# Optimization experiments

Measured on AMD Instinct MI355X. Metric: run time of the kernel, lower is better.

The kernel has to match this reference:

```python
import jax, jax.numpy as jnp
import numpy as np

B, IN, H, T = 4096, 1024, 1024, 12
TIME_PENALTY = 0.01
PONDER_EPS = 0.01


def lstm_cell(x, h, c, Wih, Whh, bih, bhh):
    # PyTorch LSTMCell: gates ordered i, f, g, o
    g = x @ Wih.T + bih + h @ Whh.T + bhh  # [B, 4H]
    i, f, gg, o = jnp.split(g, 4, axis=1)
    i = jax.nn.sigmoid(i)
    f = jax.nn.sigmoid(f)
    gg = jnp.tanh(gg)
    o = jax.nn.sigmoid(o)
    c_new = f * c + i * gg
    h_new = o * jnp.tanh(c_new)
    return h_new, c_new


def setup_inputs() -> dict:
    key = jax.random.key(0)
    ks = jax.random.split(key, 12)
    k1 = 1.0 / np.sqrt(H)
    u = lambda k, shape: jax.random.uniform(k, shape, jnp.float32, -k1, k1)
    return {
        "inputs": jax.random.normal(ks[0], (B, IN), jnp.float32),
        "W_ih1": u(ks[1], (4 * H, IN + 1)),
        "W_hh1": u(ks[2], (4 * H, H)),
        "b_ih1": u(ks[3], (4 * H,)),
        "b_hh1": u(ks[4], (4 * H,)),
        "W_ih2": u(ks[5], (4 * H, H)),
        "W_hh2": u(ks[6], (4 * H, H)),
        "b_ih2": u(ks[7], (4 * H,)),
        "b_hh2": u(ks[8], (4 * H,)),
        "W_halt": u(ks[9], (1, H)),
        "b_halt": jnp.full((1,), -1.0, jnp.float32),  # initial_halting_bias
    }


def reference(inputs, W_ih1, W_hh1, b_ih1, b_hh1, W_ih2, W_hh2, b_ih2, b_hh2, W_halt, b_halt):
    batch = inputs.shape[0]
    budget = jnp.float32(1.0 - PONDER_EPS)

    h1 = jnp.zeros((batch, H), jnp.float32)
    c1 = jnp.zeros((batch, H), jnp.float32)
    h2 = jnp.zeros((batch, H), jnp.float32)
    c2 = jnp.zeros((batch, H), jnp.float32)
    halt_accum = jnp.zeros((batch, 1), jnp.float32)
    acc_out = jnp.zeros((batch, H), jnp.float32)
    acc_rem = jnp.zeros((batch, 1), jnp.float32)
    ponder_steps = jnp.zeros((batch,), jnp.float32)
    cont = jnp.ones((batch, 1), bool)
    is_first = jnp.array(True)

    def step(carry, _):
        h1, c1, h2, c2, halt_accum, acc_out, acc_rem, ponder_steps, cont, is_first = carry
        active = jnp.any(cont)  # mimic torch's early break: inactive steps are no-ops
        flag = jnp.where(is_first, 1.0, 0.0) * jnp.ones((batch, 1), jnp.float32)
        x = jnp.concatenate([inputs, flag], axis=1)
        h1n, c1n = lstm_cell(x, h1, c1, W_ih1, W_hh1, b_ih1, b_hh1)
        act = jax.nn.relu(h1n)
        h2n, c2n = lstm_cell(act, h2, c2, W_ih2, W_hh2, b_ih2, b_hh2)
        step_halt = jax.nn.sigmoid(h2n @ W_halt.T + b_halt)  # [B,1]
        cont_f = cont.astype(jnp.float32)
        masked_halt = step_halt * cont_f
        halt_n = halt_accum + masked_halt
        ending = (halt_n > budget) & cont
        cont_n = cont & jnp.logical_not(ending)
        masked_rem = ending.astype(jnp.float32) * (1.0 - halt_n)
        acc_out_n = acc_out + (masked_halt + masked_rem) * h2n
        acc_rem_n = acc_rem + masked_halt
        ponder_n = ponder_steps + cont_n[:, 0].astype(jnp.float32)
        sel = lambda new, old: jnp.where(active, new, old)
        carry_n = (sel(h1n, h1), sel(c1n, c1), sel(h2n, h2), sel(c2n, c2),
                   sel(halt_n, halt_accum), sel(acc_out_n, acc_out),
                   sel(acc_rem_n, acc_rem), sel(ponder_n, ponder_steps),
                   jnp.where(active, cont_n, cont),
                   is_first & jnp.logical_not(active))
        return carry_n, None

    carry = (h1, c1, h2, c2, halt_accum, acc_out, acc_rem, ponder_steps, cont, is_first)
    carry, _ = jax.lax.scan(step, carry, None, length=T)
    h1, c1, h2, c2, halt_accum, acc_out, acc_rem, ponder_steps, cont, _ = carry

    # for-else branch: samples still continuing after time_limit get the remainder
    acc_out = acc_out + cont.astype(jnp.float32) * (1.0 - halt_accum) * h2
    ponder_cost = -1.0 * TIME_PENALTY * jnp.mean(acc_rem)
    return acc_out, h1, c1, h2, c2, ponder_cost, ponder_steps
```

## Files before the change

kernel.cpp:

```cpp
#include <hip/hip_runtime.h>
#include <cstdint>
#include <cstddef>


typedef _Float16 f16;
typedef f16   f16x8 __attribute__((ext_vector_type(8)));
typedef f16   f16x4 __attribute__((ext_vector_type(4)));
typedef float f32x4 __attribute__((ext_vector_type(4)));

#define TSTEPS 12

#define O_ACC   0u
#define O_H1    4194304u
#define O_C1    8388608u
#define O_H2    12582912u
#define O_C2    16777216u
#define O_PCOST 20971520u
#define O_PSTEP 20971521u

#define WS_C1    (size_t)(0u)
#define WS_C2    ((size_t)16u<<20)
#define WS_H1HI0 ((size_t)32u<<20)
#define WS_H1HI1 ((size_t)40u<<20)
#define WS_H1LO0 ((size_t)48u<<20)
#define WS_H1LO1 ((size_t)56u<<20)
#define WS_H2HI0 ((size_t)64u<<20)
#define WS_H2HI1 ((size_t)72u<<20)
#define WS_H2LO0 ((size_t)80u<<20)
#define WS_H2LO1 ((size_t)88u<<20)
#define WS_ACTHI ((size_t)96u<<20)
#define WS_ACTLO ((size_t)104u<<20)
#define WS_MISC  ((size_t)112u<<20)

#define SEC_AHI 0
#define SEC_ALO 16384
#define SEC_BHI 32768
#define SEC_BLO 49152
#define BUFSZ   65536

__device__ __forceinline__ float sigmoidf_(float x) { return 1.0f / (1.0f + expf(-x)); }

__device__ __forceinline__ void glds16(const void* g, void* l) {
    __builtin_amdgcn_global_load_lds(
        (const __attribute__((address_space(1))) unsigned int*)g,
        (__attribute__((address_space(3))) unsigned int*)l, 16, 0, 0);
}

__device__ __forceinline__ void block_tile(int& m0, int& hc0) {
    const int bid = blockIdx.x;
    const int lid = (bid & 7) * 32 + (bid >> 3);
    m0  = (lid & 15) * 256;
    hc0 = (lid >> 4) * 64;
}

template<bool B_PAIR>
__device__ __forceinline__ void pass256(
    const f16* __restrict__ Ahi, const f16* __restrict__ Alo,
    const f16* __restrict__ Bhi, const f16* __restrict__ Blo,
    const float* __restrict__ Bf32,
    int m0, int hc0, f32x4 (&acc)[8][4], char* sm)
{
    const int tid = threadIdx.x, lane = tid & 63, wid = tid >> 6;
    const int wm  = (wid >> 2) * 128;
    const int wnb = wid & 3;
    const int l15 = lane & 15, lk = lane >> 4;

    int aoff[8], boff[4];
#pragma unroll
    for (int mf = 0; mf < 8; ++mf) {
        const int row = wm + mf * 16 + l15;
        aoff[mf] = row * 64 + ((lk ^ (((row >> 1) ^ (row >> 3)) & 3)) << 4);
    }
#pragma unroll
    for (int nf = 0; nf < 4; ++nf) {
        const int lv = wnb * 64 + nf * 16 + l15;
        boff[nf] = lv * 64 + ((lk ^ (((lv >> 1) ^ (lv >> 3)) & 3)) << 4);
    }

    constexpr int NOPS = B_PAIR ? 8 : 4;
    const f16* gsrc[NOPS];
    int ldst[NOPS];
    {
        const int gl_d = lane >> 2;
        const int sl   = lane & 3;
        const int swz_gd = ((gl_d >> 1) ^ (gl_d >> 3)) & 3;
#pragma unroll
        for (int i = 0; i < NOPS; ++i) {
            const int o = wid * NOPS + i;
            const int sec = o >> 4, j = o & 15;
            const int swzv = (swz_gd ^ (2 * j)) & 3;
            const f16* base;
            size_t row;
            if (sec <= 1) { base = (sec == 0) ? Ahi : Alo; row = (size_t)(m0 + 16 * j + gl_d); }
            else {
                base = (sec == 2) ? Bhi : Blo;
                row = (size_t)((j & 3) * 1024 + hc0 + (j >> 2) * 16 + gl_d);
            }
            gsrc[i] = base + row * 1024 + ((sl ^ swzv) << 3);
            ldst[i] = sec * 16384 + j * 1024 + lane * 16;
        }
    }

    const int blv = tid >> 1;
    const int bswz = ((blv >> 1) ^ (blv >> 3)) & 3;
    const float* bsrc = nullptr;
    float4 breg[4];
    if constexpr (!B_PAIR) {
        const int wrow = ((blv >> 4) & 3) * 1024 + hc0 + (blv >> 6) * 16 + (blv & 15);
        bsrc = Bf32 + (size_t)wrow * 1024 + (tid & 1) * 16;
    }

    auto issue = [&](int i, int kt, char* buf) {
        glds16(gsrc[i] + kt * 32, buf + ldst[i]);
    };
    auto loadB = [&](int kt) {
#pragma unroll
        for (int i = 0; i < 4; ++i) breg[i] = *(const float4*)(bsrc + kt * 32 + i * 4);
    };
    auto writeB = [&](char* buf) {
#pragma unroll
        for (int i2 = 0; i2 < 2; ++i2) {
            const float4 va = breg[2 * i2], vb = breg[2 * i2 + 1];
            const f16 h0 = (f16)va.x, h1 = (f16)va.y, h2 = (f16)va.z, h3 = (f16)va.w;
            const f16 h4 = (f16)vb.x, h5 = (f16)vb.y, h6 = (f16)vb.z, h7 = (f16)vb.w;
            const f16x8 hv = {h0, h1, h2, h3, h4, h5, h6, h7};
            const f16x8 lw = {(f16)(va.x - (float)h0), (f16)(va.y - (float)h1),
                              (f16)(va.z - (float)h2), (f16)(va.w - (float)h3),
                              (f16)(vb.x - (float)h4), (f16)(vb.y - (float)h5),
                              (f16)(vb.z - (float)h6), (f16)(vb.w - (float)h7)};
            const int slot = ((tid & 1) * 2 + i2) ^ bswz;
            const int off = blv * 64 + (slot << 4);
            *(f16x8*)(buf + SEC_BHI + off) = hv;
            *(f16x8*)(buf + SEC_BLO + off) = lw;
        }
    };

    constexpr int IST_P[5] = {0, 3, 6, 8, 8};
    constexpr int IST_M[5] = {0, 2, 3, 4, 4};

#pragma unroll
    for (int i = 0; i < NOPS; ++i) issue(i, 0, sm);
    if constexpr (!B_PAIR) {
        loadB(0);
        asm volatile("s_waitcnt vmcnt(0)" ::: "memory");
        writeB(sm);
    }
    asm volatile("s_waitcnt vmcnt(0) lgkmcnt(0)" ::: "memory");
    __builtin_amdgcn_s_barrier();
    asm volatile("" ::: "memory");

    int cur = 0;
#pragma unroll 1
    for (int kt = 0; kt < 32; ++kt) {
        char* bc = sm + cur * BUFSZ;
        char* bn = sm + (cur ^ 1) * BUFSZ;
        const bool pre = (kt < 31);
        f16x8 bh[4], bl[4];
#pragma unroll
        for (int p = 0; p < 4; ++p) {
            f16x8 ah0 = *(const f16x8*)(bc + SEC_AHI + aoff[2 * p]);
            f16x8 ah1 = *(const f16x8*)(bc + SEC_AHI + aoff[2 * p + 1]);
            f16x8 al0 = *(const f16x8*)(bc + SEC_ALO + aoff[2 * p]);
            f16x8 al1 = *(const f16x8*)(bc + SEC_ALO + aoff[2 * p + 1]);
            if (p == 0) {
#pragma unroll
                for (int nf = 0; nf < 4; ++nf) {
                    bh[nf] = *(const f16x8*)(bc + SEC_BHI + boff[nf]);
                    bl[nf] = *(const f16x8*)(bc + SEC_BLO + boff[nf]);
                }
            }
            if (pre) {
                if constexpr (B_PAIR) {
#pragma unroll
                    for (int i = IST_P[p]; i < IST_P[p + 1]; ++i) issue(i, kt + 1, bn);
                } else {
#pragma unroll
                    for (int i = IST_M[p]; i < IST_M[p + 1]; ++i) issue(i, kt + 1, bn);
                    if (p == 0) loadB(kt + 1);
                }
            }
            __builtin_amdgcn_s_barrier();
            __builtin_amdgcn_s_setprio(1);
#pragma unroll
            for (int i = 0; i < 2; ++i) {
                const f16x8 xh = i ? ah1 : ah0;
                const f16x8 xl = i ? al1 : al0;
#pragma unroll
                for (int nf = 0; nf < 4; ++nf) {
                    acc[2 * p + i][nf] = __builtin_amdgcn_mfma_f32_16x16x32_f16(xh, bh[nf], acc[2 * p + i][nf], 0, 0, 0);
                    acc[2 * p + i][nf] = __builtin_amdgcn_mfma_f32_16x16x32_f16(xh, bl[nf], acc[2 * p + i][nf], 0, 0, 0);
                    acc[2 * p + i][nf] = __builtin_amdgcn_mfma_f32_16x16x32_f16(xl, bh[nf], acc[2 * p + i][nf], 0, 0, 0);
                }
            }
            __builtin_amdgcn_s_setprio(0);
            if (p < 3) __builtin_amdgcn_s_barrier();
        }
        asm volatile("s_waitcnt vmcnt(0)" ::: "memory");
        if constexpr (!B_PAIR) { if (pre) writeB(bn); }
        asm volatile("s_waitcnt lgkmcnt(0)" ::: "memory");
        __builtin_amdgcn_s_barrier();
        asm volatile("" ::: "memory");
        cur ^= 1;
    }
}

__global__ __launch_bounds__(512) void k_z1(
    const f16* __restrict__ xhi, const f16* __restrict__ xlo,
    const f16* __restrict__ W1hi, const f16* __restrict__ W1lo,
    const float* __restrict__ bih1, const float* __restrict__ bhh1,
    float* __restrict__ Z1)
{
    __shared__ __align__(16) char sm[2 * BUFSZ];
    int m0, hc0; block_tile(m0, hc0);
    f32x4 acc[8][4];
#pragma unroll
    for (int a = 0; a < 8; ++a)
#pragma unroll
        for (int b = 0; b < 4; ++b) acc[a][b] = (f32x4){0.f, 0.f, 0.f, 0.f};
    pass256<true>(xhi, xlo, W1hi, W1lo, nullptr, m0, hc0, acc, sm);

    const int tid = threadIdx.x, lane = tid & 63, wid = tid >> 6;
    const int wm = (wid >> 2) * 128, wnb = wid & 3, l15 = lane & 15, lk = lane >> 4;
    const int hc = hc0 + wnb * 16 + l15;
#pragma unroll
    for (int mf = 0; mf < 8; ++mf)
#pragma unroll
        for (int r = 0; r < 4; ++r) {
            const int row = m0 + wm + mf * 16 + lk * 4 + r;
#pragma unroll
            for (int g = 0; g < 4; ++g) {
                const int R = g * 1024 + hc;
                Z1[(size_t)row * 4096 + R] = acc[mf][g][r] + bih1[R] + bhh1[R];
            }
        }
}

__global__ __launch_bounds__(512) void k_stepA(
    const float* __restrict__ Z1, const float* __restrict__ Whh1,
    const f16* __restrict__ h1hi_in, const f16* __restrict__ h1lo_in,
    const float* __restrict__ flagcol, float* __restrict__ c1,
    f16* __restrict__ h1hi_out, f16* __restrict__ h1lo_out,
    f16* __restrict__ acthi, f16* __restrict__ actlo,
    const unsigned* __restrict__ cnt_prev, int step)
{
    if (step > 0 && cnt_prev[0] == 0u) return;
    __shared__ __align__(16) char sm[2 * BUFSZ];
    int m0, hc0; block_tile(m0, hc0);
    f32x4 acc[8][4];
#pragma unroll
    for (int a = 0; a < 8; ++a)
#pragma unroll
        for (int b = 0; b < 4; ++b) acc[a][b] = (f32x4){0.f, 0.f, 0.f, 0.f};
    if (step > 0)
        pass256<false>(h1hi_in, h1lo_in, nullptr, nullptr, Whh1, m0, hc0, acc, sm);

    const int tid = threadIdx.x, lane = tid & 63, wid = tid >> 6;
    const int wm = (wid >> 2) * 128, wnb = wid & 3, l15 = lane & 15, lk = lane >> 4;
    const int hc = hc0 + wnb * 16 + l15;
#pragma unroll
    for (int mf = 0; mf < 8; ++mf)
#pragma unroll
        for (int r = 0; r < 4; ++r) {
            const int row = m0 + wm + mf * 16 + lk * 4 + r;
            float p[4];
#pragma unroll
            for (int g = 0; g < 4; ++g) {
                const int R = g * 1024 + hc;
                p[g] = acc[mf][g][r] + Z1[(size_t)row * 4096 + R];
                if (step == 0) p[g] += flagcol[R];
            }
            const float ig = sigmoidf_(p[0]);
            const float fg = sigmoidf_(p[1]);
            const float gg = tanhf(p[2]);
            const float og = sigmoidf_(p[3]);
            const int idx = row * 1024 + hc;
            const float cold = (step == 0) ? 0.0f : c1[idx];
            const float cn = fg * cold + ig * gg;
            c1[idx] = cn;
            const float h = og * tanhf(cn);
            const f16 hh = (f16)h;
            const f16 hl = (f16)(h - (float)hh);
            h1hi_out[idx] = hh; h1lo_out[idx] = hl;
            const bool pos = h > 0.0f;
            acthi[idx] = pos ? hh : (f16)0.0f;
            actlo[idx] = pos ? hl : (f16)0.0f;
        }
}

__global__ __launch_bounds__(512) void k_stepB(
    const f16* __restrict__ acthi, const f16* __restrict__ actlo,
    const float* __restrict__ Wih2,
    const f16* __restrict__ h2hi_in, const f16* __restrict__ h2lo_in,
    const float* __restrict__ Whh2,
    const float* __restrict__ bih2, const float* __restrict__ bhh2,
    float* __restrict__ c2, f16* __restrict__ h2hi_out, f16* __restrict__ h2lo_out,
    const unsigned* __restrict__ cnt_prev, int step)
{
    if (step > 0 && cnt_prev[0] == 0u) return;
    __shared__ __align__(16) char sm[2 * BUFSZ];
    int m0, hc0; block_tile(m0, hc0);
    f32x4 acc[8][4];
#pragma unroll
    for (int a = 0; a < 8; ++a)
#pragma unroll
        for (int b = 0; b < 4; ++b) acc[a][b] = (f32x4){0.f, 0.f, 0.f, 0.f};
    pass256<false>(acthi, actlo, nullptr, nullptr, Wih2, m0, hc0, acc, sm);
    if (step > 0)
        pass256<false>(h2hi_in, h2lo_in, nullptr, nullptr, Whh2, m0, hc0, acc, sm);

    const int tid = threadIdx.x, lane = tid & 63, wid = tid >> 6;
    const int wm = (wid >> 2) * 128, wnb = wid & 3, l15 = lane & 15, lk = lane >> 4;
    const int hc = hc0 + wnb * 16 + l15;
#pragma unroll
    for (int mf = 0; mf < 8; ++mf)
#pragma unroll
        for (int r = 0; r < 4; ++r) {
            const int row = m0 + wm + mf * 16 + lk * 4 + r;
            float p[4];
#pragma unroll
            for (int g = 0; g < 4; ++g) {
                const int R = g * 1024 + hc;
                p[g] = acc[mf][g][r] + bih2[R] + bhh2[R];
            }
            const float ig = sigmoidf_(p[0]);
            const float fg = sigmoidf_(p[1]);
            const float gg = tanhf(p[2]);
            const float og = sigmoidf_(p[3]);
            const int idx = row * 1024 + hc;
            const float cold = (step == 0) ? 0.0f : c2[idx];
            const float cn = fg * cold + ig * gg;
            c2[idx] = cn;
            const float h = og * tanhf(cn);
            const f16 hh = (f16)h;
            h2hi_out[idx] = hh;
            h2lo_out[idx] = (f16)(h - (float)hh);
        }
}

__global__ __launch_bounds__(256) void k_haltacc(
    const f16* __restrict__ h2hi, const f16* __restrict__ h2lo,
    const float* __restrict__ Whalt, const float* __restrict__ bhalt,
    float* __restrict__ halt, float* __restrict__ cont,
    float* __restrict__ ponder_out, unsigned* __restrict__ ctrl,
    float* __restrict__ acc_out,
    const unsigned* __restrict__ cnt_prev, int step)
{
    if (step > 0 && cnt_prev[0] == 0u) return;
    const int lane = threadIdx.x & 63;
    const int b = blockIdx.x * 4 + (threadIdx.x >> 6);
    const size_t base = (size_t)b * 1024;
    float sum = 0.0f;
    for (int k = lane; k < 1024; k += 64)
        sum += ((float)h2hi[base + k] + (float)h2lo[base + k]) * Whalt[k];
#pragma unroll
    for (int off = 32; off > 0; off >>= 1) sum += __shfl_down(sum, off, 64);
    float co = 0.0f;
    if (lane == 0) {
        const float sh = sigmoidf_(sum + bhalt[0]);
        if (cont[b] != 0.0f) {
            const float hn = halt[b] + sh;
            const bool ending = hn > 0.99f;
            co = sh + (ending ? (1.0f - hn) : 0.0f);
            halt[b] = hn;
            if (!ending) {
                ponder_out[b] += 1.0f;
                atomicAdd(&ctrl[step], 1u);
            } else {
                cont[b] = 0.0f;
            }
        }
        if (b == 0) ctrl[12] = (unsigned)(step + 1);
    }
    co = __shfl(co, 0, 64);
    if (step == 0 || co != 0.0f) {
        float4* dst = (float4*)(acc_out + base);
        const f16x4* hi4 = (const f16x4*)(h2hi + base);
        const f16x4* lo4 = (const f16x4*)(h2lo + base);
#pragma unroll
        for (int j = 0; j < 4; ++j) {
            const int i = lane + 64 * j;
            const f16x4 hv = hi4[i];
            const f16x4 lv = lo4[i];
            float4 d = (step == 0) ? (float4){0.f, 0.f, 0.f, 0.f} : dst[i];
            d.x = fmaf(co, (float)hv[0] + (float)lv[0], d.x);
            d.y = fmaf(co, (float)hv[1] + (float)lv[1], d.y);
            d.z = fmaf(co, (float)hv[2] + (float)lv[2], d.z);
            d.w = fmaf(co, (float)hv[3] + (float)lv[3], d.w);
            dst[i] = d;
        }
    }
}

__global__ __launch_bounds__(256) void k_small_init(
    float* __restrict__ halt, float* __restrict__ cont,
    float* __restrict__ ponder_out, unsigned* __restrict__ ctrl)
{
    const int b = blockIdx.x * 256 + threadIdx.x;
    if (b < 4096) { halt[b] = 0.0f; cont[b] = 1.0f; ponder_out[b] = 0.0f; }
    if (b < 16) ctrl[b] = 0u;
}

__global__ __launch_bounds__(256) void k_split_flat(
    const float* __restrict__ src, f16* __restrict__ hi, f16* __restrict__ lo)
{
    const size_t i = ((size_t)blockIdx.x * 256 + threadIdx.x) * 4;
    const float4 v = *(const float4*)(src + i);
    const f16 s0 = (f16)v.x, s1 = (f16)v.y, s2 = (f16)v.z, s3 = (f16)v.w;
    const f16x4 hv = {s0, s1, s2, s3};
    const f16x4 lw = {(f16)(v.x - (float)s0), (f16)(v.y - (float)s1),
                      (f16)(v.z - (float)s2), (f16)(v.w - (float)s3)};
    *(f16x4*)(hi + i) = hv;
    *(f16x4*)(lo + i) = lw;
}

__global__ __launch_bounds__(256) void k_split_wih1(
    const float* __restrict__ src, f16* __restrict__ hi, f16* __restrict__ lo,
    float* __restrict__ flagcol)
{
    const int t = blockIdx.x * 256 + threadIdx.x;
    const int row = t >> 8, c4 = (t & 255) << 2;
    const float* s = src + (size_t)row * 1025 + c4;
    const float v0 = s[0], v1 = s[1], v2 = s[2], v3 = s[3];
    const f16 s0 = (f16)v0, s1 = (f16)v1, s2 = (f16)v2, s3 = (f16)v3;
    const f16x4 hv = {s0, s1, s2, s3};
    const f16x4 lw = {(f16)(v0 - (float)s0), (f16)(v1 - (float)s1),
                      (f16)(v2 - (float)s2), (f16)(v3 - (float)s3)};
    const size_t di = (size_t)row * 1024 + c4;
    *(f16x4*)(hi + di) = hv;
    *(f16x4*)(lo + di) = lw;
    if ((t & 255) == 0) flagcol[row] = src[(size_t)row * 1025 + 1024];
}

__global__ __launch_bounds__(256) void k_fin1(
    const f16* __restrict__ h1hi0, const f16* __restrict__ h1hi1,
    const f16* __restrict__ h1lo0, const f16* __restrict__ h1lo1,
    const f16* __restrict__ h2hi0, const f16* __restrict__ h2hi1,
    const f16* __restrict__ h2lo0, const f16* __restrict__ h2lo1,
    const float* __restrict__ c1s, const float* __restrict__ c2s,
    const float* __restrict__ halt, const float* __restrict__ cont,
    const unsigned* __restrict__ ctrl, float* __restrict__ out)
{
    const int par = (int)(ctrl[12] & 1u);
    const f16* h1h = par ? h1hi1 : h1hi0;
    const f16* h1l = par ? h1lo1 : h1lo0;
    const f16* h2h = par ? h2hi1 : h2hi0;
    const f16* h2l = par ? h2lo1 : h2lo0;
    const int b = blockIdx.x;
    const float rem = (cont[b] != 0.0f) ? (1.0f - halt[b]) : 0.0f;
    const int base = b * 1024;
    for (int i = threadIdx.x; i < 1024; i += 256) {
        const float h1v = (float)h1h[base + i] + (float)h1l[base + i];
        const float h2v = (float)h2h[base + i] + (float)h2l[base + i];
        out[O_H1 + base + i] = h1v;
        out[O_C1 + base + i] = c1s[base + i];
        out[O_H2 + base + i] = h2v;
        out[O_C2 + base + i] = c2s[base + i];
        if (rem != 0.0f) out[O_ACC + base + i] += rem * h2v;
    }
}

__global__ __launch_bounds__(256) void k_fin2(
    const float* __restrict__ halt, float* __restrict__ out)
{
    __shared__ float red[256];
    float s = 0.0f;
    for (int i = threadIdx.x; i < 4096; i += 256) s += halt[i];
    red[threadIdx.x] = s;
    __syncthreads();
    for (int w = 128; w > 0; w >>= 1) {
        if (threadIdx.x < w) red[threadIdx.x] += red[threadIdx.x + w];
        __syncthreads();
    }
    if (threadIdx.x == 0) out[O_PCOST] = -0.01f * (red[0] * (1.0f / 4096.0f));
}

extern "C" void kernel_launch(void* const* d_in, const int* in_sizes, int n_in,
                              void* d_out, int out_size, void* d_ws, size_t ws_size,
                              hipStream_t stream) {
    const float* inputs = (const float*)d_in[0];
    const float* W_ih1  = (const float*)d_in[1];
    const float* W_hh1  = (const float*)d_in[2];
    const float* b_ih1  = (const float*)d_in[3];
    const float* b_hh1  = (const float*)d_in[4];
    const float* W_ih2  = (const float*)d_in[5];
    const float* W_hh2  = (const float*)d_in[6];
    const float* b_ih2  = (const float*)d_in[7];
    const float* b_hh2  = (const float*)d_in[8];
    const float* W_halt = (const float*)d_in[9];
    const float* b_halt = (const float*)d_in[10];

    float* out = (float*)d_out;
    float* Z1  = out + O_H1;

    char* wsb = (char*)d_ws;
    float* c1s = (float*)(wsb + WS_C1);
    float* c2s = (float*)(wsb + WS_C2);
    f16* h1hi[2] = { (f16*)(wsb + WS_H1HI0), (f16*)(wsb + WS_H1HI1) };
    f16* h1lo[2] = { (f16*)(wsb + WS_H1LO0), (f16*)(wsb + WS_H1LO1) };
    f16* h2hi[2] = { (f16*)(wsb + WS_H2HI0), (f16*)(wsb + WS_H2HI1) };
    f16* h2lo[2] = { (f16*)(wsb + WS_H2LO0), (f16*)(wsb + WS_H2LO1) };
    f16* acthi   = (f16*)(wsb + WS_ACTHI);
    f16* actlo   = (f16*)(wsb + WS_ACTLO);
    float* halt    = (float*)(wsb + WS_MISC);
    float* cont    = halt + 4096;
    float* coef    = cont + 4096;
    float* flagcol = coef + 4096;
    unsigned* ctrl = (unsigned*)(flagcol + 4096);

    f16* xhi  = h1hi[0]; f16* xlo  = h1lo[0];
    f16* W1hi = h2hi[0]; f16* W1lo = h2lo[0];

    k_small_init<<<16, 256, 0, stream>>>(halt, cont, out + O_PSTEP, ctrl);

    k_split_wih1<<<4096, 256, 0, stream>>>(W_ih1, W1hi, W1lo, flagcol);
    k_split_flat<<<4096, 256, 0, stream>>>(inputs, xhi, xlo);
    k_z1<<<256, 512, 0, stream>>>(xhi, xlo, W1hi, W1lo, b_ih1, b_hh1, Z1);

    for (int s = 0; s < TSTEPS; ++s) {
        const int wsel = (s & 1) ? 0 : 1;
        const int rsel = 1 - wsel;
        const unsigned* cnt_prev = ctrl + (s > 0 ? s - 1 : 0);

        k_stepA<<<256, 512, 0, stream>>>(Z1, W_hh1, h1hi[rsel], h1lo[rsel],
                                         flagcol, c1s,
                                         h1hi[wsel], h1lo[wsel], acthi, actlo,
                                         cnt_prev, s);
        k_stepB<<<256, 512, 0, stream>>>(acthi, actlo, W_ih2,
                                         h2hi[rsel], h2lo[rsel], W_hh2,
                                         b_ih2, b_hh2, c2s,
                                         h2hi[wsel], h2lo[wsel],
                                         cnt_prev, s);
        k_haltacc<<<1024, 256, 0, stream>>>(h2hi[wsel], h2lo[wsel], W_halt, b_halt,
                                            halt, cont, out + O_PSTEP, ctrl,
                                            out + O_ACC, cnt_prev, s);
    }

    k_fin1<<<4096, 256, 0, stream>>>(h1hi[0], h1hi[1], h1lo[0], h1lo[1],
                                     h2hi[0], h2hi[1], h2lo[0], h2lo[1],
                                     c1s, c2s, halt, cont, ctrl, out);
    k_fin2<<<1, 256, 0, stream>>>(halt, out);
}
```

Baseline: 1.476 ms.

## Load B fragments straight into registers and use K=64 tiles for GEMM passes

The GEMM main loop is restructured. The K tile grows from 32 to 64, so there are 16 iterations instead of 32. B (weight) fragments are no longer staged through LDS: each wave loads its weight rows directly from global memory into registers and converts fp32 to hi/lo fp16 in registers. Only A goes through LDS, using a new XOR swizzle. This removes the LDS writes, reads and barriers for B, plus the per-subphase barriers. In exchange each wave now reloads B redundantly (the two M-halves share no B), register pressure rises, and the setprio hints are dropped.

```diff
diff --git a/kernel.cpp b/kernel.cpp
--- a/kernel.cpp
+++ b/kernel.cpp
@@ -32,10 +32,7 @@
 #define WS_ACTLO ((size_t)104u<<20)
 #define WS_MISC  ((size_t)112u<<20)
 
-#define SEC_AHI 0
-#define SEC_ALO 16384
-#define SEC_BHI 32768
-#define SEC_BLO 49152
+#define SEC_ALO 32768
 #define BUFSZ   65536
 
 __device__ __forceinline__ float sigmoidf_(float x) { return 1.0f / (1.0f + expf(-x)); }
@@ -54,7 +51,7 @@
 }
 
 template<bool B_PAIR>
-__device__ __forceinline__ void pass256(
+__device__ __forceinline__ void passK64(
     const f16* __restrict__ Ahi, const f16* __restrict__ Alo,
     const f16* __restrict__ Bhi, const f16* __restrict__ Blo,
     const float* __restrict__ Bf32,
@@ -65,142 +62,127 @@
     const int wnb = wid & 3;
     const int l15 = lane & 15, lk = lane >> 4;
 
-    int aoff[8], boff[4];
+    int rbase[8], rx[8];
 #pragma unroll
     for (int mf = 0; mf < 8; ++mf) {
         const int row = wm + mf * 16 + l15;
-        aoff[mf] = row * 64 + ((lk ^ (((row >> 1) ^ (row >> 3)) & 3)) << 4);
-    }
+        rbase[mf] = row * 128;
+        rx[mf]    = row & 7;
+    }
+
+    const f16* ga[8];
+    int albase[8];
+    {
+        const int rl = lane >> 3, sl = lane & 7;
+        const int gchunk = (sl ^ rl) * 8;
+#pragma unroll
+        for (int i = 0; i < 8; ++i) {
+            const int o = wid * 8 + i;
+            const int sec = o >> 5, j = o & 31;
+            const f16* base = (sec == 0) ? Ahi : Alo;
+            ga[i] = base + (size_t)(m0 + j * 8 + rl) * 1024 + gchunk;
+            albase[i] = sec * SEC_ALO + j * 1024;
+        }
+    }
+
+    const int wrow0 = hc0 + wnb * 16 + l15;
+    const float* pB32[4];
+    const f16*   pBh[4];
+    const f16*   pBl[4];
 #pragma unroll
     for (int nf = 0; nf < 4; ++nf) {
-        const int lv = wnb * 64 + nf * 16 + l15;
-        boff[nf] = lv * 64 + ((lk ^ (((lv >> 1) ^ (lv >> 3)) & 3)) << 4);
-    }
-
-    constexpr int NOPS = B_PAIR ? 8 : 4;
-    const f16* gsrc[NOPS];
-    int ldst[NOPS];
-    {
-        const int gl_d = lane >> 2;
-        const int sl   = lane & 3;
-        const int swz_gd = ((gl_d >> 1) ^ (gl_d >> 3)) & 3;
-#pragma unroll
-        for (int i = 0; i < NOPS; ++i) {
-            const int o = wid * NOPS + i;
-            const int sec = o >> 4, j = o & 15;
-            const int swzv = (swz_gd ^ (2 * j)) & 3;
-            const f16* base;
-            size_t row;
-            if (sec <= 1) { base = (sec == 0) ? Ahi : Alo; row = (size_t)(m0 + 16 * j + gl_d); }
-            else {
-                base = (sec == 2) ? Bhi : Blo;
-                row = (size_t)((j & 3) * 1024 + hc0 + (j >> 2) * 16 + gl_d);
-            }
-            gsrc[i] = base + row * 1024 + ((sl ^ swzv) << 3);
-            ldst[i] = sec * 16384 + j * 1024 + lane * 16;
-        }
-    }
-
-    const int blv = tid >> 1;
-    const int bswz = ((blv >> 1) ^ (blv >> 3)) & 3;
-    const float* bsrc = nullptr;
-    float4 breg[4];
-    if constexpr (!B_PAIR) {
-        const int wrow = ((blv >> 4) & 3) * 1024 + hc0 + (blv >> 6) * 16 + (blv & 15);
-        bsrc = Bf32 + (size_t)wrow * 1024 + (tid & 1) * 16;
-    }
-
-    auto issue = [&](int i, int kt, char* buf) {
-        glds16(gsrc[i] + kt * 32, buf + ldst[i]);
+        const size_t ro = (size_t)(nf * 1024 + wrow0) * 1024 + lk * 8;
+        if constexpr (B_PAIR) { pBh[nf] = Bhi + ro; pBl[nf] = Blo + ro; }
+        else                  { pB32[nf] = Bf32 + ro; }
+    }
+
+    float4 breg[4][2][2];
+    int4   bregh[4][2], bregl[4][2];
+
+    auto issueA = [&](int kt, char* buf) {
+#pragma unroll
+        for (int i = 0; i < 8; ++i)
+            glds16(ga[i] + kt * 64, buf + albase[i]);
     };
-    auto loadB = [&](int kt) {
-#pragma unroll
-        for (int i = 0; i < 4; ++i) breg[i] = *(const float4*)(bsrc + kt * 32 + i * 4);
+    auto issueB = [&](int kt) {
+#pragma unroll
+        for (int nf = 0; nf < 4; ++nf)
+#pragma unroll
+            for (int ks = 0; ks < 2; ++ks) {
+                if constexpr (B_PAIR) {
+                    bregh[nf][ks] = *(const int4*)(pBh[nf] + kt * 64 + ks * 32);
+                    bregl[nf][ks] = *(const int4*)(pBl[nf] + kt * 64 + ks * 32);
+                } else {
+                    const float* p = pB32[nf] + kt * 64 + ks * 32;
+                    breg[nf][ks][0] = *(const float4*)(p);
+                    breg[nf][ks][1] = *(const float4*)(p + 4);
+                }
+            }
     };
-    auto writeB = [&](char* buf) {
-#pragma unroll
-        for (int i2 = 0; i2 < 2; ++i2) {
-            const float4 va = breg[2 * i2], vb = breg[2 * i2 + 1];
-            const f16 h0 = (f16)va.x, h1 = (f16)va.y, h2 = (f16)va.z, h3 = (f16)va.w;
-            const f16 h4 = (f16)vb.x, h5 = (f16)vb.y, h6 = (f16)vb.z, h7 = (f16)vb.w;
-            const f16x8 hv = {h0, h1, h2, h3, h4, h5, h6, h7};
-            const f16x8 lw = {(f16)(va.x - (float)h0), (f16)(va.y - (float)h1),
-                              (f16)(va.z - (float)h2), (f16)(va.w - (float)h3),
-                              (f16)(vb.x - (float)h4), (f16)(vb.y - (float)h5),
-                              (f16)(vb.z - (float)h6), (f16)(vb.w - (float)h7)};
-            const int slot = ((tid & 1) * 2 + i2) ^ bswz;
-            const int off = blv * 64 + (slot << 4);
-            *(f16x8*)(buf + SEC_BHI + off) = hv;
-            *(f16x8*)(buf + SEC_BLO + off) = lw;
-        }
-    };
-
-    constexpr int IST_P[5] = {0, 3, 6, 8, 8};
-    constexpr int IST_M[5] = {0, 2, 3, 4, 4};
-
-#pragma unroll
-    for (int i = 0; i < NOPS; ++i) issue(i, 0, sm);
-    if constexpr (!B_PAIR) {
-        loadB(0);
-        asm volatile("s_waitcnt vmcnt(0)" ::: "memory");
-        writeB(sm);
-    }
-    asm volatile("s_waitcnt vmcnt(0) lgkmcnt(0)" ::: "memory");
+
+    issueA(0, sm);
+    issueB(0);
+    asm volatile("s_waitcnt vmcnt(0)" ::: "memory");
     __builtin_amdgcn_s_barrier();
     asm volatile("" ::: "memory");
 
-    int cur = 0;
 #pragma unroll 1
-    for (int kt = 0; kt < 32; ++kt) {
-        char* bc = sm + cur * BUFSZ;
-        char* bn = sm + (cur ^ 1) * BUFSZ;
-        const bool pre = (kt < 31);
-        f16x8 bh[4], bl[4];
-#pragma unroll
-        for (int p = 0; p < 4; ++p) {
-            f16x8 ah0 = *(const f16x8*)(bc + SEC_AHI + aoff[2 * p]);
-            f16x8 ah1 = *(const f16x8*)(bc + SEC_AHI + aoff[2 * p + 1]);
-            f16x8 al0 = *(const f16x8*)(bc + SEC_ALO + aoff[2 * p]);
-            f16x8 al1 = *(const f16x8*)(bc + SEC_ALO + aoff[2 * p + 1]);
-            if (p == 0) {
-#pragma unroll
-                for (int nf = 0; nf < 4; ++nf) {
-                    bh[nf] = *(const f16x8*)(bc + SEC_BHI + boff[nf]);
-                    bl[nf] = *(const f16x8*)(bc + SEC_BLO + boff[nf]);
+    for (int kt = 0; kt < 16; ++kt) {
+        char* bc = sm + (kt & 1) * BUFSZ;
+        char* bn = sm + ((kt + 1) & 1) * BUFSZ;
+        const bool pre = (kt < 15);
+
+        if (pre) issueA(kt + 1, bn);
+
+        f16x8 bh[4][2], bl[4][2];
+#pragma unroll
+        for (int nf = 0; nf < 4; ++nf)
+#pragma unroll
+            for (int ks = 0; ks < 2; ++ks) {
+                if constexpr (B_PAIR) {
+                    bh[nf][ks] = *(const f16x8*)&bregh[nf][ks];
+                    bl[nf][ks] = *(const f16x8*)&bregl[nf][ks];
+                } else {
+                    const float* f0 = (const float*)&breg[nf][ks][0];
+                    const float* f1 = (const float*)&breg[nf][ks][1];
+                    f16x8 h, l;
+#pragma unroll
+                    for (int j = 0; j < 4; ++j) {
+                        const f16 a = (f16)f0[j];
+                        h[j] = a; l[j] = (f16)(f0[j] - (float)a);
+                        const f16 b = (f16)f1[j];
+                        h[4 + j] = b; l[4 + j] = (f16)(f1[j] - (float)b);
+                    }
+                    bh[nf][ks] = h; bl[nf][ks] = l;
                 }
             }
-            if (pre) {
-                if constexpr (B_PAIR) {
-#pragma unroll
-                    for (int i = IST_P[p]; i < IST_P[p + 1]; ++i) issue(i, kt + 1, bn);
-                } else {
-#pragma unroll
-                    for (int i = IST_M[p]; i < IST_M[p + 1]; ++i) issue(i, kt + 1, bn);
-                    if (p == 0) loadB(kt + 1);
+
+        if (pre) issueB(kt + 1);
+
+#pragma unroll
+        for (int ks = 0; ks < 2; ++ks) {
+            f16x8 ah[8], al[8];
+#pragma unroll
+            for (int mf = 0; mf < 8; ++mf) {
+                const int off = rbase[mf] + ((((ks << 2) | lk) ^ rx[mf]) << 4);
+                ah[mf] = *(const f16x8*)(bc + off);
+                al[mf] = *(const f16x8*)(bc + SEC_ALO + off);
+            }
+#pragma unroll
+            for (int nf = 0; nf < 4; ++nf)
+#pragma unroll
+                for (int mf = 0; mf < 8; ++mf) {
+                    acc[mf][nf] = __builtin_amdgcn_mfma_f32_16x16x32_f16(ah[mf], bh[nf][ks], acc[mf][nf], 0, 0, 0);
+                    acc[mf][nf] = __builtin_amdgcn_mfma_f32_16x16x32_f16(ah[mf], bl[nf][ks], acc[mf][nf], 0, 0, 0);
+                    acc[mf][nf] = __builtin_amdgcn_mfma_f32_16x16x32_f16(al[mf], bh[nf][ks], acc[mf][nf], 0, 0, 0);
                 }
-            }
+        }
+
+        asm volatile("s_waitcnt vmcnt(0)" ::: "memory");
+        if (pre) {
             __builtin_amdgcn_s_barrier();
-            __builtin_amdgcn_s_setprio(1);
-#pragma unroll
-            for (int i = 0; i < 2; ++i) {
-                const f16x8 xh = i ? ah1 : ah0;
-                const f16x8 xl = i ? al1 : al0;
-#pragma unroll
-                for (int nf = 0; nf < 4; ++nf) {
-                    acc[2 * p + i][nf] = __builtin_amdgcn_mfma_f32_16x16x32_f16(xh, bh[nf], acc[2 * p + i][nf], 0, 0, 0);
-                    acc[2 * p + i][nf] = __builtin_amdgcn_mfma_f32_16x16x32_f16(xh, bl[nf], acc[2 * p + i][nf], 0, 0, 0);
-                    acc[2 * p + i][nf] = __builtin_amdgcn_mfma_f32_16x16x32_f16(xl, bh[nf], acc[2 * p + i][nf], 0, 0, 0);
-                }
-            }
-            __builtin_amdgcn_s_setprio(0);
-            if (p < 3) __builtin_amdgcn_s_barrier();
-        }
-        asm volatile("s_waitcnt vmcnt(0)" ::: "memory");
-        if constexpr (!B_PAIR) { if (pre) writeB(bn); }
-        asm volatile("s_waitcnt lgkmcnt(0)" ::: "memory");
-        __builtin_amdgcn_s_barrier();
-        asm volatile("" ::: "memory");
-        cur ^= 1;
+            asm volatile("" ::: "memory");
+        }
     }
 }
 
@@ -217,7 +199,7 @@
     for (int a = 0; a < 8; ++a)
 #pragma unroll
         for (int b = 0; b < 4; ++b) acc[a][b] = (f32x4){0.f, 0.f, 0.f, 0.f};
-    pass256<true>(xhi, xlo, W1hi, W1lo, nullptr, m0, hc0, acc, sm);
+    passK64<true>(xhi, xlo, W1hi, W1lo, nullptr, m0, hc0, acc, sm);
 
     const int tid = threadIdx.x, lane = tid & 63, wid = tid >> 6;
     const int wm = (wid >> 2) * 128, wnb = wid & 3, l15 = lane & 15, lk = lane >> 4;
@@ -252,7 +234,7 @@
 #pragma unroll
         for (int b = 0; b < 4; ++b) acc[a][b] = (f32x4){0.f, 0.f, 0.f, 0.f};
     if (step > 0)
-        pass256<false>(h1hi_in, h1lo_in, nullptr, nullptr, Whh1, m0, hc0, acc, sm);
+        passK64<false>(h1hi_in, h1lo_in, nullptr, nullptr, Whh1, m0, hc0, acc, sm);
 
     const int tid = threadIdx.x, lane = tid & 63, wid = tid >> 6;
     const int wm = (wid >> 2) * 128, wnb = wid & 3, l15 = lane & 15, lk = lane >> 4;
@@ -304,9 +286,9 @@
     for (int a = 0; a < 8; ++a)
 #pragma unroll
         for (int b = 0; b < 4; ++b) acc[a][b] = (f32x4){0.f, 0.f, 0.f, 0.f};
-    pass256<false>(acthi, actlo, nullptr, nullptr, Wih2, m0, hc0, acc, sm);
+    passK64<false>(acthi, actlo, nullptr, nullptr, Wih2, m0, hc0, acc, sm);
     if (step > 0)
-        pass256<false>(h2hi_in, h2lo_in, nullptr, nullptr, Whh2, m0, hc0, acc, sm);
+        passK64<false>(h2hi_in, h2lo_in, nullptr, nullptr, Whh2, m0, hc0, acc, sm);
 
     const int tid = threadIdx.x, lane = tid & 63, wid = tid >> 6;
     const int wm = (wid >> 2) * 128, wnb = wid & 3, l15 = lane & 15, lk = lane >> 4;
```

New measurement: 5.008 ms. +239.3%, slower.
